# Optimization experiments

Measured on AMD Instinct MI355X. Metric: run time of the kernel, lower is better.

Reference implementation:

```python
import jax, jax.numpy as jnp
import numpy as np

B, T, E, V, U = 32, 250, 256, 10000, 1024  # batch, seq, embed, vocab, units


def lstm_cell(x, h, c, k, rk, b):
    """Keras LSTMCell math: gates ordered i, f, g(candidate), o."""
    z = x @ k + h @ rk + b  # [B, 4U]
    i, f, g, o = jnp.split(z, 4, axis=-1)
    i = jax.nn.sigmoid(i)
    f = jax.nn.sigmoid(f)
    g = jnp.tanh(g)
    o = jax.nn.sigmoid(o)
    c_next = f * c + i * g
    h_next = o * jnp.tanh(c_next)
    return h_next, c_next


def setup_inputs() -> dict:
    key = jax.random.key(0)
    ks = jax.random.split(key, 8)
    s = 0.05
    return {
        "tokens": jax.random.randint(ks[0], (B, T), 0, V, dtype=jnp.int32),
        "emb": jax.random.normal(ks[1], (V, E), dtype=jnp.float32) * s,
        "k0": jax.random.normal(ks[2], (E, 4 * U), dtype=jnp.float32) * s,
        "rk0": jax.random.normal(ks[3], (U, 4 * U), dtype=jnp.float32) * s,
        "b0": jnp.zeros((4 * U,), dtype=jnp.float32),
        "k1": jax.random.normal(ks[4], (E, 4 * U), dtype=jnp.float32) * s,
        "rk1": jax.random.normal(ks[5], (U, 4 * U), dtype=jnp.float32) * s,
        "b1": jnp.zeros((4 * U,), dtype=jnp.float32),
        "wout": jax.random.normal(ks[6], (2 * U, 1), dtype=jnp.float32) * s,
        "bout": jnp.zeros((1,), dtype=jnp.float32),
    }


def reference(tokens, emb, k0, rk0, b0, k1, rk1, b1, wout, bout):
    x = emb[tokens]  # [B, T, E]

    # LSTM cell 0: scan over all T timesteps from zero state.
    def step(carry, xt):
        h, c = carry
        h2, c2 = lstm_cell(xt, h, c, k0, rk0, b0)
        return (h2, c2), None

    zero = jnp.zeros((B, U), dtype=x.dtype)
    (h0, _), _ = jax.lax.scan(step, (zero, zero), jnp.swapaxes(x, 0, 1))

    # LSTM cell 1: the original loops over x[:, -1:, :] -> exactly one step.
    h1, _ = lstm_cell(x[:, -1, :], zero, zero, k1, rk1, b1)

    logits = jnp.concatenate([h0, h1], axis=1) @ wout + bout  # [B, 1]
    return jax.nn.sigmoid(logits)
```

## Files before the change

### kernel.cpp

```cpp
#include <hip/hip_runtime.h>
#include <cmath>

#define B_  32
#define T_  250
#define E_  256
#define U_  1024
#define FU_ 4096
#define VK_ 1280
#define NT_ 40

typedef __attribute__((ext_vector_type(8)))  __bf16 bf16x8;
typedef __attribute__((ext_vector_type(4)))  float  f32x4;

__device__ __forceinline__ float sigf(float x) { return 1.f / (1.f + __expf(-x)); }

__global__ __launch_bounds__(256) void wsplit_kernel(
    const float* __restrict__ rk0, const float* __restrict__ k0,
    __bf16* __restrict__ wfh)
{
    __shared__ float tile[32][65];
    const int tid = threadIdx.x;
    const int jt  = blockIdx.x & 63;
    const int kt  = blockIdx.x >> 6;
    const int gk0 = kt * 32;
    const int j0  = jt * 64;

    {
        const int c = tid & 63, r4 = tid >> 6;
        #pragma unroll
        for (int i = 0; i < 8; ++i) {
            const int r  = r4 * 8 + i;
            const int gk = gk0 + r;
            const float* src = (gk < U_) ? (rk0 + (size_t)gk * FU_ + j0 + c)
                                         : (k0 + (size_t)(gk - U_) * FU_ + j0 + c);
            tile[r][c] = *src;
        }
    }
    __syncthreads();
    {
        const int j_loc = tid >> 2, kseg = tid & 3;
        bf16x8 hi;
        #pragma unroll
        for (int i = 0; i < 8; ++i)
            hi[i] = (__bf16)tile[kseg * 8 + i][j_loc];
        const int col = j0 + j_loc;
        const int g   = col >> 10;
        const int u   = col & 1023;
        const int bi  = u >> 2;
        const int c   = g * 4 + (u & 3);
        const int l   = kseg * 16 + c;
        const size_t off = (((size_t)bi * NT_ + kt) * 64 + l) * 8;
        *(bf16x8*)(wfh + off) = hi;
    }
}

__global__ __launch_bounds__(256) void xsplit_all(
    const int* __restrict__ tokens, const float* __restrict__ emb,
    __bf16* __restrict__ xf)
{
    const int t   = blockIdx.x;
    const int tid = threadIdx.x;
    const int b   = tid >> 3;
    const int kc  = (tid & 7) * 32;
    const int tok = tokens[b * T_ + t];
    const float* ep = emb + (size_t)tok * E_ + kc;
    const int Kx = kc >> 5;
    const int mt = b >> 4;
    #pragma unroll
    for (int g8 = 0; g8 < 4; ++g8) {
        bf16x8 hi;
        #pragma unroll
        for (int j = 0; j < 8; ++j) hi[j] = (__bf16)ep[g8 * 8 + j];
        const int lane2 = g8 * 16 + (b & 15);
        const size_t off = ((((size_t)t * 8 + Kx) * 2 + mt) * 64 + lane2) * 8;
        *(bf16x8*)(xf + off) = hi;
    }
}

__global__ __launch_bounds__(512) void step_fused(
    const __bf16* __restrict__ wfh,
    const float* __restrict__ b0,
    const __bf16* __restrict__ af_r, __bf16* __restrict__ af_w,
    const __bf16* __restrict__ xf,
    float* __restrict__ c_st, int t)
{
    __shared__ float part[8][32][18];

    const int tid  = threadIdx.x;
    const int lane = tid & 63;
    const int kq   = tid >> 6;
    const int bi   = blockIdx.x;

    const __bf16* wbh = wfh + ((size_t)bi * NT_) * 512 + lane * 8;
    const __bf16* xft = xf + ((size_t)t * 8 * 2) * 512;

    f32x4 acc0 = {}, acc1 = {};

    #pragma unroll
    for (int s = 0; s < 5; ++s) {
        const int K = kq * 5 + s;
        const bf16x8 wh = *(const bf16x8*)(wbh + (size_t)K * 512);
        const __bf16* abase = (K < 32)
            ? (af_r + ((size_t)(K * 2) * 64 + lane) * 8)
            : (xft + ((size_t)((K - 32) * 2) * 64 + lane) * 8);
        const bf16x8 a0 = *(const bf16x8*)abase;
        const bf16x8 a1 = *(const bf16x8*)(abase + 512);
        acc0 = __builtin_amdgcn_mfma_f32_16x16x32_bf16(a0, wh, acc0, 0, 0, 0);
        acc1 = __builtin_amdgcn_mfma_f32_16x16x32_bf16(a1, wh, acc1, 0, 0, 0);
    }

    #pragma unroll
    for (int r = 0; r < 4; ++r) {
        const int rr = (lane >> 4) * 4 + r;
        part[kq][rr][lane & 15]      = acc0[r];
        part[kq][16 + rr][lane & 15] = acc1[r];
    }
    __syncthreads();

    if (tid < 128) {
        const int b  = tid >> 2, uu = tid & 3;
        const int u0 = bi * 4;
        float z[4];
        #pragma unroll
        for (int g = 0; g < 4; ++g) {
            const int c = g * 4 + uu;
            float s2 = b0[g * U_ + u0 + uu];
            #pragma unroll
            for (int q = 0; q < 8; ++q) s2 += part[q][b][c];
            z[g] = s2;
        }
        const float ii = sigf(z[0]), ff = sigf(z[1]);
        const float gg = tanhf(z[2]), oo = sigf(z[3]);
        const int ci = b * U_ + u0 + uu;
        const float cv = ff * c_st[ci] + ii * gg;
        c_st[ci] = cv;
        const float hv = oo * tanhf(cv);
        const int u = u0 + uu;
        const size_t fo = ((size_t)((u >> 5) * 2 + (b >> 4)) * 64
                           + ((u >> 3) & 3) * 16 + (b & 15)) * 8 + (u & 7);
        af_w[fo] = (__bf16)hv;
    }
}

__global__ __launch_bounds__(256) void cell1_gemm(
    const int* __restrict__ tokens, const float* __restrict__ emb,
    const float* __restrict__ k1, const float* __restrict__ b1,
    float* __restrict__ Pc)
{
    const int tid  = threadIdx.x;
    const int lane = tid & 63;
    const int warp = tid >> 6;
    const int j  = blockIdx.x;
    const int ct = j & 15, bg = j >> 4;
    const int b  = bg * 4 + warp;
    const int col = ct * 256 + lane * 4;
    const int tok = tokens[b * T_ + (T_ - 1)];
    const float* wp = k1 + col;
    const float* xp = emb + (size_t)tok * E_;
    float4 acc = *reinterpret_cast<const float4*>(b1 + col);
    #pragma unroll 4
    for (int k4 = 0; k4 < 64; ++k4) {
        const float4 x4 = *reinterpret_cast<const float4*>(xp + k4 * 4);
        const float4 w0 = *reinterpret_cast<const float4*>(wp + (size_t)(k4 * 4 + 0) * FU_);
        const float4 w1 = *reinterpret_cast<const float4*>(wp + (size_t)(k4 * 4 + 1) * FU_);
        const float4 w2 = *reinterpret_cast<const float4*>(wp + (size_t)(k4 * 4 + 2) * FU_);
        const float4 w3 = *reinterpret_cast<const float4*>(wp + (size_t)(k4 * 4 + 3) * FU_);
        acc.x = fmaf(x4.x, w0.x, acc.x); acc.y = fmaf(x4.x, w0.y, acc.y);
        acc.z = fmaf(x4.x, w0.z, acc.z); acc.w = fmaf(x4.x, w0.w, acc.w);
        acc.x = fmaf(x4.y, w1.x, acc.x); acc.y = fmaf(x4.y, w1.y, acc.y);
        acc.z = fmaf(x4.y, w1.z, acc.z); acc.w = fmaf(x4.y, w1.w, acc.w);
        acc.x = fmaf(x4.z, w2.x, acc.x); acc.y = fmaf(x4.z, w2.y, acc.y);
        acc.z = fmaf(x4.z, w2.z, acc.z); acc.w = fmaf(x4.z, w2.w, acc.w);
        acc.x = fmaf(x4.w, w3.x, acc.x); acc.y = fmaf(x4.w, w3.y, acc.y);
        acc.z = fmaf(x4.w, w3.z, acc.z); acc.w = fmaf(x4.w, w3.w, acc.w);
    }
    *reinterpret_cast<float4*>(Pc + (size_t)b * FU_ + col) = acc;
}

__global__ __launch_bounds__(256) void final_kernel(
    const __bf16* __restrict__ hfh,
    const float* __restrict__ Pc,
    const float* __restrict__ wout, const float* __restrict__ bout,
    float* __restrict__ out)
{
    const int b = blockIdx.x;
    const int tid = threadIdx.x;
    float s = 0.f;
    for (int u = tid; u < U_; u += 256) {
        const size_t fo = ((size_t)((u >> 5) * 2 + (b >> 4)) * 64
                           + ((u >> 3) & 3) * 16 + (b & 15)) * 8 + (u & 7);
        const float h0v = (float)hfh[fo];
        const float zi = Pc[(size_t)b * FU_ + u];
        const float zg = Pc[(size_t)b * FU_ + 2 * U_ + u];
        const float zo = Pc[(size_t)b * FU_ + 3 * U_ + u];
        const float c1 = sigf(zi) * tanhf(zg);
        const float h1 = sigf(zo) * tanhf(c1);
        s += h0v * wout[u] + h1 * wout[U_ + u];
    }
    #pragma unroll
    for (int off = 32; off > 0; off >>= 1) s += __shfl_down(s, off, 64);
    __shared__ float partf[4];
    if ((tid & 63) == 0) partf[tid >> 6] = s;
    __syncthreads();
    if (tid == 0) {
        const float tot = partf[0] + partf[1] + partf[2] + partf[3] + bout[0];
        out[b] = 1.f / (1.f + __expf(-tot));
    }
}

extern "C" void kernel_launch(void* const* d_in, const int* in_sizes, int n_in,
                              void* d_out, int out_size, void* d_ws, size_t ws_size,
                              hipStream_t stream) {
    const int*   tokens = (const int*)  d_in[0];
    const float* emb    = (const float*)d_in[1];
    const float* k0     = (const float*)d_in[2];
    const float* rk0    = (const float*)d_in[3];
    const float* b0     = (const float*)d_in[4];
    const float* k1     = (const float*)d_in[5];
    const float* b1     = (const float*)d_in[7];
    const float* wout   = (const float*)d_in[8];
    const float* bout   = (const float*)d_in[9];
    float* out = (float*)d_out;

    const size_t BU   = (size_t)B_ * U_;
    const size_t BFU  = (size_t)B_ * FU_;
    const size_t AFSZ = (size_t)32 * 2 * 64 * 8;
    const size_t XFSZ = (size_t)T_ * 8 * 2 * 64 * 8;
    const size_t WSZ  = (size_t)FU_ * VK_;

    float*  c    = (float*)d_ws;
    __bf16* af0  = (__bf16*)(c + BU);
    __bf16* af1  = af0 + AFSZ;
    __bf16* xf   = af1 + AFSZ;
    __bf16* wfh  = xf + XFSZ;
    float*  Pc   = (float*)(wfh + WSZ);

    hipMemsetAsync(c, 0, BU * sizeof(float) + AFSZ * sizeof(__bf16), stream);

    wsplit_kernel<<<2560, 256, 0, stream>>>(rk0, k0, wfh);
    xsplit_all<<<T_, 256, 0, stream>>>(tokens, emb, xf);
    cell1_gemm<<<128, 256, 0, stream>>>(tokens, emb, k1, b1, Pc);

    for (int t = 0; t < T_; ++t) {
        const __bf16* ar = (t & 1) ? af1 : af0;
        __bf16*       aw = (t & 1) ? af0 : af1;
        step_fused<<<256, 512, 0, stream>>>(wfh, b0, ar, aw, xf, c, t);
    }

    final_kernel<<<B_, 256, 0, stream>>>(af0, Pc, wout, bout, out);
}
```

Measured before the change: 1.126 ms.

## Give each step block 8 units instead of 4, halving blocks and reusing A fragments

The per-step LSTM kernel now computes 8 hidden units (32 gate columns) per block instead of 4. Each A fragment (h and x) is reused across two weight column tiles with four MFMAs per k-step, and the grid is halved to 128 blocks. The weight pre-layout is changed to match, and tanhf is replaced by an exp-based fast tanh. Fewer blocks cut redundant activation loads but leave about half of the CUs idle on a latency-bound recurrent step, and the fast tanh slightly changes numerics.

Measured after the change: 1.163 ms. 1.03x slower.

```diff
diff --git a/kernel.cpp b/kernel.cpp
--- a/kernel.cpp
+++ b/kernel.cpp
@@ -8,11 +8,13 @@
 #define FU_ 4096
 #define VK_ 1280
 #define NT_ 40
+#define NB_ 128
 
 typedef __attribute__((ext_vector_type(8)))  __bf16 bf16x8;
 typedef __attribute__((ext_vector_type(4)))  float  f32x4;
 
-__device__ __forceinline__ float sigf(float x) { return 1.f / (1.f + __expf(-x)); }
+__device__ __forceinline__ float sigf(float x)  { return 1.f / (1.f + __expf(-x)); }
+__device__ __forceinline__ float tanhfast(float x) { return 1.f - 2.f / (1.f + __expf(2.f * x)); }
 
 __global__ __launch_bounds__(256) void wsplit_kernel(
     const float* __restrict__ rk0, const float* __restrict__ k0,
@@ -46,10 +48,12 @@
         const int col = j0 + j_loc;
         const int g   = col >> 10;
         const int u   = col & 1023;
-        const int bi  = u >> 2;
-        const int c   = g * 4 + (u & 3);
-        const int l   = kseg * 16 + c;
-        const size_t off = (((size_t)bi * NT_ + kt) * 64 + l) * 8;
+        const int bi  = u >> 3;
+        const int cl  = g * 8 + (u & 7);
+        const int cf  = cl >> 4;
+        const int cc  = cl & 15;
+        const int l   = kseg * 16 + cc;
+        const size_t off = ((((size_t)bi * NT_ + kt) * 2 + cf) * 64 + l) * 8;
         *(bf16x8*)(wfh + off) = hi;
     }
 }
@@ -84,58 +88,64 @@
     const __bf16* __restrict__ xf,
     float* __restrict__ c_st, int t)
 {
-    __shared__ float part[8][32][18];
+    __shared__ float part[8][32][34];
 
     const int tid  = threadIdx.x;
     const int lane = tid & 63;
     const int kq   = tid >> 6;
     const int bi   = blockIdx.x;
 
-    const __bf16* wbh = wfh + ((size_t)bi * NT_) * 512 + lane * 8;
+    const __bf16* wb  = wfh + ((size_t)bi * NT_ * 2) * 512 + lane * 8;
     const __bf16* xft = xf + ((size_t)t * 8 * 2) * 512;
 
-    f32x4 acc0 = {}, acc1 = {};
+    f32x4 acc00 = {}, acc01 = {}, acc10 = {}, acc11 = {};
 
     #pragma unroll
     for (int s = 0; s < 5; ++s) {
         const int K = kq * 5 + s;
-        const bf16x8 wh = *(const bf16x8*)(wbh + (size_t)K * 512);
-        const __bf16* abase = (K < 32)
+        const bf16x8 w0 = *(const bf16x8*)(wb + ((size_t)K * 2 + 0) * 512);
+        const bf16x8 w1 = *(const bf16x8*)(wb + ((size_t)K * 2 + 1) * 512);
+        const __bf16* ab = (K < 32)
             ? (af_r + ((size_t)(K * 2) * 64 + lane) * 8)
             : (xft + ((size_t)((K - 32) * 2) * 64 + lane) * 8);
-        const bf16x8 a0 = *(const bf16x8*)abase;
-        const bf16x8 a1 = *(const bf16x8*)(abase + 512);
-        acc0 = __builtin_amdgcn_mfma_f32_16x16x32_bf16(a0, wh, acc0, 0, 0, 0);
-        acc1 = __builtin_amdgcn_mfma_f32_16x16x32_bf16(a1, wh, acc1, 0, 0, 0);
+        const bf16x8 a0 = *(const bf16x8*)ab;
+        const bf16x8 a1 = *(const bf16x8*)(ab + 512);
+        acc00 = __builtin_amdgcn_mfma_f32_16x16x32_bf16(a0, w0, acc00, 0, 0, 0);
+        acc01 = __builtin_amdgcn_mfma_f32_16x16x32_bf16(a0, w1, acc01, 0, 0, 0);
+        acc10 = __builtin_amdgcn_mfma_f32_16x16x32_bf16(a1, w0, acc10, 0, 0, 0);
+        acc11 = __builtin_amdgcn_mfma_f32_16x16x32_bf16(a1, w1, acc11, 0, 0, 0);
     }
 
     #pragma unroll
     for (int r = 0; r < 4; ++r) {
         const int rr = (lane >> 4) * 4 + r;
-        part[kq][rr][lane & 15]      = acc0[r];
-        part[kq][16 + rr][lane & 15] = acc1[r];
+        const int cc = lane & 15;
+        part[kq][rr][cc]           = acc00[r];
+        part[kq][rr][16 + cc]      = acc01[r];
+        part[kq][16 + rr][cc]      = acc10[r];
+        part[kq][16 + rr][16 + cc] = acc11[r];
     }
     __syncthreads();
 
-    if (tid < 128) {
-        const int b  = tid >> 2, uu = tid & 3;
-        const int u0 = bi * 4;
+    if (tid < 256) {
+        const int b  = tid >> 3, ul = tid & 7;
+        const int u0 = bi * 8;
         float z[4];
         #pragma unroll
         for (int g = 0; g < 4; ++g) {
-            const int c = g * 4 + uu;
-            float s2 = b0[g * U_ + u0 + uu];
+            const int cl = g * 8 + ul;
+            float s2 = b0[g * U_ + u0 + ul];
             #pragma unroll
-            for (int q = 0; q < 8; ++q) s2 += part[q][b][c];
+            for (int q = 0; q < 8; ++q) s2 += part[q][b][cl];
             z[g] = s2;
         }
         const float ii = sigf(z[0]), ff = sigf(z[1]);
-        const float gg = tanhf(z[2]), oo = sigf(z[3]);
-        const int ci = b * U_ + u0 + uu;
+        const float gg = tanhfast(z[2]), oo = sigf(z[3]);
+        const int ci = b * U_ + u0 + ul;
         const float cv = ff * c_st[ci] + ii * gg;
         c_st[ci] = cv;
-        const float hv = oo * tanhf(cv);
-        const int u = u0 + uu;
+        const float hv = oo * tanhfast(cv);
+        const int u = u0 + ul;
         const size_t fo = ((size_t)((u >> 5) * 2 + (b >> 4)) * 64
                            + ((u >> 3) & 3) * 16 + (b & 15)) * 8 + (u & 7);
         af_w[fo] = (__bf16)hv;
@@ -244,7 +254,7 @@
     for (int t = 0; t < T_; ++t) {
         const __bf16* ar = (t & 1) ? af1 : af0;
         __bf16*       aw = (t & 1) ? af0 : af1;
-        step_fused<<<256, 512, 0, stream>>>(wfh, b0, ar, aw, xf, c, t);
+        step_fused<<<NB_, 512, 0, stream>>>(wfh, b0, ar, aw, xf, c, t);
     }
 
     final_kernel<<<B_, 256, 0, stream>>>(af0, Pc, wout, bout, out);
```
